# Performance work log

Measured on AMD Instinct MI355X. Metric: run time of the kernel, lower is better.

The kernel has to match this reference:

```python
import jax, jax.numpy as jnp
import numpy as np

NBIT = 8
QMAX = 2 ** (NBIT - 1) - 1  # 127, symmetric 8-bit range


def _sym_scale(x):
    # symmetric_linear_quantization_params: scale = max|x| / (2^(b-1)-1)
    return jnp.max(jnp.abs(x)) / QMAX


def setup_inputs() -> dict:
    key = jax.random.key(0)
    k1, k2, k3 = jax.random.split(key, 3)
    B, DIN, DOUT = 8192, 2048, 8192
    x = jax.random.normal(k1, (B, DIN), jnp.float32)
    weight = jax.random.normal(k2, (DOUT, DIN), jnp.float32) * 0.02
    bias = jax.random.normal(k3, (DOUT,), jnp.float32) * 0.01
    return {"x": x, "weight": weight, "bias": bias}


def reference(x, weight, bias):
    # --- QuantAct 1: symmetric 8-bit activation quantization ---
    s_a = _sym_scale(x)                                   # scalar act scale
    x_int = jnp.clip(jnp.round(x / s_a), -QMAX, QMAX)     # int8 values in fp32
    # --- QuantLinear: per-output-channel 8-bit weight quant + integer GEMM ---
    s_w = jnp.max(jnp.abs(weight), axis=1) / QMAX         # [DOUT] weight scales
    w_int = jnp.clip(jnp.round(weight / s_w[:, None]), -QMAX, QMAX)
    s_b = s_w * s_a                                        # output/bias scale [DOUT]
    b_int = jnp.round(bias / s_b)
    out_int = x_int @ w_int.T + b_int                      # [B, DOUT] int accumulation
    out = out_int * s_b                                    # dequantize
    # --- QuantAct 2: requantize output, symmetric 8-bit ---
    s_o = _sym_scale(out)
    out_q = jnp.clip(jnp.round(out / s_o), -QMAX, QMAX) * s_o
    return out_q
```

## Files before the change

### kernel.cpp

```cpp
#include <hip/hip_runtime.h>
#include <stdint.h>

#define B_DIM 8192
#define DIN   2048
#define DOUT  8192
#define NKT   (DIN / 128)

typedef int  v4i __attribute__((ext_vector_type(4)));
typedef char c8  __attribute__((ext_vector_type(8)));

__device__ __forceinline__ void gload_lds16(const void* g, void* l) {
  __builtin_amdgcn_global_load_lds(
      (const __attribute__((address_space(1))) void*)g,
      (__attribute__((address_space(3))) void*)l, 16, 0, 0);
}

__device__ __forceinline__ float wave_max(float m) {
#pragma unroll
  for (int off = 32; off; off >>= 1) m = fmaxf(m, __shfl_xor(m, off, 64));
  return m;
}

__global__ void k_init(unsigned int* p) {
  p[0] = 0u;
  p[1] = 0u;
}

__global__ __launch_bounds__(256) void k_absmax(const float4* __restrict__ x,
                                                int n4,
                                                unsigned int* __restrict__ out_bits) {
  int idx = blockIdx.x * blockDim.x + threadIdx.x;
  int stride = gridDim.x * blockDim.x;
  float m = 0.f;
  for (int i = idx; i < n4; i += stride) {
    float4 v = x[i];
    m = fmaxf(m, fabsf(v.x));
    m = fmaxf(m, fabsf(v.y));
    m = fmaxf(m, fabsf(v.z));
    m = fmaxf(m, fabsf(v.w));
  }
  m = wave_max(m);
  __shared__ float red[4];
  if ((threadIdx.x & 63) == 0) red[threadIdx.x >> 6] = m;
  __syncthreads();
  if (threadIdx.x == 0) {
    m = fmaxf(fmaxf(red[0], red[1]), fmaxf(red[2], red[3]));
    atomicMax(out_bits, __float_as_uint(m));
  }
}

__global__ void k_quant_x(const float* __restrict__ x, c8* __restrict__ xq,
                          int n8, const unsigned int* __restrict__ sa_bits) {
  int i = blockIdx.x * blockDim.x + threadIdx.x;
  if (i >= n8) return;
  float s_a = __uint_as_float(*sa_bits) / 127.0f;
  const float4* p = (const float4*)(x + (size_t)i * 8);
  float4 v0 = p[0], v1 = p[1];
  float vv[8] = {v0.x, v0.y, v0.z, v0.w, v1.x, v1.y, v1.z, v1.w};
  c8 q;
#pragma unroll
  for (int j = 0; j < 8; ++j) {
    float r = fminf(fmaxf(rintf(vv[j] / s_a), -127.f), 127.f);
    q[j] = (char)(int)r;
  }
  xq[i] = q;
}

__global__ __launch_bounds__(256) void k_quant_w(const float* __restrict__ w,
                                                 c8* __restrict__ wq,
                                                 float* __restrict__ s_w) {
  int row = blockIdx.x;
  int tid = threadIdx.x;
  const float4* wr = (const float4*)(w + (size_t)row * DIN);
  float4 v0 = wr[tid * 2], v1 = wr[tid * 2 + 1];
  float vv[8] = {v0.x, v0.y, v0.z, v0.w, v1.x, v1.y, v1.z, v1.w};
  float m = 0.f;
#pragma unroll
  for (int j = 0; j < 8; ++j) m = fmaxf(m, fabsf(vv[j]));
  m = wave_max(m);
  __shared__ float wmax[4];
  if ((tid & 63) == 0) wmax[tid >> 6] = m;
  __syncthreads();
  m = fmaxf(fmaxf(wmax[0], wmax[1]), fmaxf(wmax[2], wmax[3]));
  float s = m / 127.0f;
  if (tid == 0) s_w[row] = s;
  c8 q;
#pragma unroll
  for (int j = 0; j < 8; ++j) {
    float r = fminf(fmaxf(rintf(vv[j] / s), -127.f), 127.f);
    q[j] = (char)(int)r;
  }
  wq[(size_t)row * (DIN / 8) + tid] = q;
}

__global__ __launch_bounds__(512, 2) void k_gemm8(
    const char* __restrict__ Aq, const char* __restrict__ Bq,
    const float* __restrict__ s_w, const float* __restrict__ bias,
    const unsigned int* __restrict__ sa_bits, float* __restrict__ out,
    unsigned int* __restrict__ omax_bits) {
  __shared__ __align__(16) char lds[131072];

  const int tid = threadIdx.x;
  const int lane = tid & 63;
  const int wave = tid >> 6;
  const int wm = wave >> 2;
  const int wn = wave & 3;

  const int orig = blockIdx.x;
  const int xcd = orig & 7;
  const int k = orig >> 3;
  const int bx = (xcd & 3) * 8 + (k & 7);
  const int by = (xcd >> 2) * 16 + (k >> 3);
  const int row0 = by * 256, col0 = bx * 256;

  const int srow = ((tid >> 6) << 4) | (tid & 15);
  const int skb = tid & 48;
  const char* aS = Aq + (size_t)(row0 + srow) * DIN + skb;
  const char* bS = Bq + (size_t)(col0 + srow) * DIN + skb;

  auto STAGE = [&](int kt, int ks) {
    if (kt >= NKT) kt -= 2;
    int slot = kt & 1;
    const char* srcA = aS + (size_t)kt * 128 + ks * 64;
    const char* srcB = bS + (size_t)kt * 128 + ks * 64;
    int dstA = slot * 65536 + ks * 16384 + tid * 16;
    gload_lds16(srcA, &lds[dstA]);
    gload_lds16(srcA + (size_t)128 * DIN, &lds[dstA + 8192]);
    gload_lds16(srcB, &lds[dstA + 32768]);
    gload_lds16(srcB + (size_t)128 * DIN, &lds[dstA + 40960]);
  };

  v4i acc[2][4][4];
#pragma unroll
  for (int mh = 0; mh < 2; ++mh)
#pragma unroll
    for (int mf = 0; mf < 4; ++mf)
#pragma unroll
      for (int nf = 0; nf < 4; ++nf) acc[mh][mf][nf] = (v4i){0, 0, 0, 0};

  const int lb = lane * 16;
  v4i b0[4], al0[4], b1[4], al1[4];

#define PHASE(CSLOT, CKS, CUR_B, CUR_AL, NSLOT, NKS, NXT_B, NXT_AL, SKT, SKS) \
  do {                                                                        \
    asm volatile("s_waitcnt vmcnt(4)" ::: "memory");                          \
    asm volatile("s_barrier" ::: "memory");                                   \
    STAGE(SKT, SKS);                                                          \
    const int nb = (NSLOT)*65536 + (NKS)*16384;                               \
    _Pragma("unroll") for (int nf = 0; nf < 4; ++nf) NXT_B[nf] =              \
        *(const v4i*)&lds[nb + 32768 + (wn * 4 + nf) * 1024 + lb];            \
    _Pragma("unroll") for (int mf = 0; mf < 4; ++mf) NXT_AL[mf] =             \
        *(const v4i*)&lds[nb + (wm * 8 + mf) * 1024 + lb];                    \
    const int cb = (CSLOT)*65536 + (CKS)*16384;                               \
    v4i ah[4];                                                                \
    _Pragma("unroll") for (int mf = 0; mf < 4; ++mf) ah[mf] =                 \
        *(const v4i*)&lds[cb + (wm * 8 + 4 + mf) * 1024 + lb];                \
    __builtin_amdgcn_s_setprio(1);                                            \
    _Pragma("unroll") for (int mf = 0; mf < 4; ++mf)                          \
        _Pragma("unroll") for (int nf = 0; nf < 4; ++nf) acc[0][mf][nf] =     \
        __builtin_amdgcn_mfma_i32_16x16x64_i8(CUR_AL[mf], CUR_B[nf],          \
                                              acc[0][mf][nf], 0, 0, 0);       \
    _Pragma("unroll") for (int mf = 0; mf < 4; ++mf)                          \
        _Pragma("unroll") for (int nf = 0; nf < 4; ++nf) acc[1][mf][nf] =     \
        __builtin_amdgcn_mfma_i32_16x16x64_i8(ah[mf], CUR_B[nf],              \
                                              acc[1][mf][nf], 0, 0, 0);       \
    __builtin_amdgcn_s_setprio(0);                                            \
  } while (0)

  STAGE(0, 0);
  STAGE(0, 1);
  STAGE(1, 0);
  asm volatile("s_waitcnt vmcnt(8)" ::: "memory");
  asm volatile("s_barrier" ::: "memory");
#pragma unroll
  for (int nf = 0; nf < 4; ++nf)
    b0[nf] = *(const v4i*)&lds[32768 + (wn * 4 + nf) * 1024 + lb];
#pragma unroll
  for (int mf = 0; mf < 4; ++mf)
    al0[mf] = *(const v4i*)&lds[(wm * 8 + mf) * 1024 + lb];

#pragma unroll 1
  for (int i = 0; i < NKT / 2; ++i) {
    PHASE(0, 0, b0, al0, 0, 1, b1, al1, 2 * i + 1, 1);
    PHASE(0, 1, b1, al1, 1, 0, b0, al0, 2 * i + 2, 0);
    PHASE(1, 0, b0, al0, 1, 1, b1, al1, 2 * i + 2, 1);
    PHASE(1, 1, b1, al1, 0, 0, b0, al0, 2 * i + 3, 0);
  }
#undef PHASE

  const int fr = lane & 15;
  float s_a = __uint_as_float(*sa_bits) / 127.0f;
  float lmax = 0.f;
#pragma unroll
  for (int nf = 0; nf < 4; ++nf) {
    int col = col0 + wn * 64 + nf * 16 + fr;
    float sw = s_w[col];
    float sb = sw * s_a;
    float bint = rintf(bias[col] / sb);
#pragma unroll
    for (int mh = 0; mh < 2; ++mh)
#pragma unroll
      for (int mf = 0; mf < 4; ++mf) {
        int rbase = row0 + wm * 128 + mh * 64 + mf * 16 + (lane >> 4) * 4;
#pragma unroll
        for (int r = 0; r < 4; ++r) {
          float o = ((float)acc[mh][mf][nf][r] + bint) * sb;
          out[(size_t)(rbase + r) * DOUT + col] = o;
          lmax = fmaxf(lmax, fabsf(o));
        }
      }
  }
  lmax = wave_max(lmax);
  asm volatile("s_waitcnt vmcnt(0)" ::: "memory");
  __syncthreads();
  float* red = (float*)lds;
  if (lane == 0) red[wave] = lmax;
  __syncthreads();
  if (tid == 0) {
    float m = 0.f;
#pragma unroll
    for (int w2 = 0; w2 < 8; ++w2) m = fmaxf(m, red[w2]);
    atomicMax(omax_bits, __float_as_uint(m));
  }
}

__global__ void k_requant(float4* __restrict__ out, int n4,
                          const unsigned int* __restrict__ omax_bits) {
  float s_o = __uint_as_float(*omax_bits) / 127.0f;
  int idx = blockIdx.x * blockDim.x + threadIdx.x;
  int stride = gridDim.x * blockDim.x;
  for (int i = idx; i < n4; i += stride) {
    float4 v = out[i];
    v.x = fminf(fmaxf(rintf(v.x / s_o), -127.f), 127.f) * s_o;
    v.y = fminf(fmaxf(rintf(v.y / s_o), -127.f), 127.f) * s_o;
    v.z = fminf(fmaxf(rintf(v.z / s_o), -127.f), 127.f) * s_o;
    v.w = fminf(fmaxf(rintf(v.w / s_o), -127.f), 127.f) * s_o;
    out[i] = v;
  }
}

extern "C" void kernel_launch(void* const* d_in, const int* in_sizes, int n_in,
                              void* d_out, int out_size, void* d_ws,
                              size_t ws_size, hipStream_t stream) {
  const float* x = (const float*)d_in[0];
  const float* w = (const float*)d_in[1];
  const float* bias = (const float*)d_in[2];
  float* out = (float*)d_out;
  char* ws = (char*)d_ws;

  unsigned int* absbits = (unsigned int*)ws;
  float* s_w = (float*)(ws + 512);
  char* xq = ws + 65536;
  char* wq = ws + 65536 + (size_t)B_DIM * DIN;

  k_init<<<1, 1, 0, stream>>>(absbits);
  k_absmax<<<1024, 256, 0, stream>>>((const float4*)x, B_DIM * DIN / 4, absbits);
  k_quant_x<<<(B_DIM * DIN / 8) / 256, 256, 0, stream>>>(x, (c8*)xq,
                                                         B_DIM * DIN / 8, absbits);
  k_quant_w<<<DOUT, 256, 0, stream>>>(w, (c8*)wq, s_w);
  k_gemm8<<<1024, 512, 0, stream>>>(xq, wq, s_w, bias, absbits, out, absbits + 1);
  k_requant<<<4096, 256, 0, stream>>>((float4*)out, B_DIM * DOUT / 4, absbits + 1);
}
```

Before: 345.6 us.

## Replace pipelined 256x256 int8 GEMM with simple single-buffered 128x128 tile kernel

The hand-pipelined, double-buffered 256x256-tile int8 GEMM is replaced with a plain 128x128-tile kernel of 256 threads and a 32KB LDS buffer. Each k-step loads into LDS, synchronises, then runs the MFMAs, with no overlap between loads and compute. The intent is to raise occupancy and simplify scheduling, but it loses the software pipelining and halves data reuse per tile, which raises global traffic and adds barrier stalls.

```diff
diff --git a/kernel.cpp b/kernel.cpp
--- a/kernel.cpp
+++ b/kernel.cpp
@@ -93,100 +93,71 @@
   wq[(size_t)row * (DIN / 8) + tid] = q;
 }
 
-__global__ __launch_bounds__(512, 2) void k_gemm8(
+__global__ __launch_bounds__(256, 3) void k_gemm(
     const char* __restrict__ Aq, const char* __restrict__ Bq,
     const float* __restrict__ s_w, const float* __restrict__ bias,
     const unsigned int* __restrict__ sa_bits, float* __restrict__ out,
     unsigned int* __restrict__ omax_bits) {
-  __shared__ __align__(16) char lds[131072];
+  __shared__ __align__(16) char lds[32768];
 
   const int tid = threadIdx.x;
   const int lane = tid & 63;
   const int wave = tid >> 6;
-  const int wm = wave >> 2;
-  const int wn = wave & 3;
+  const int wm = wave >> 1;
+  const int wn = wave & 1;
 
   const int orig = blockIdx.x;
   const int xcd = orig & 7;
   const int k = orig >> 3;
-  const int bx = (xcd & 3) * 8 + (k & 7);
-  const int by = (xcd >> 2) * 16 + (k >> 3);
-  const int row0 = by * 256, col0 = bx * 256;
+  const int bx = (xcd & 3) * 16 + (k & 15);
+  const int by = (xcd >> 2) * 32 + (k >> 4);
+  const int row0 = by * 128, col0 = bx * 128;
 
   const int srow = ((tid >> 6) << 4) | (tid & 15);
   const int skb = tid & 48;
   const char* aS = Aq + (size_t)(row0 + srow) * DIN + skb;
   const char* bS = Bq + (size_t)(col0 + srow) * DIN + skb;
 
-  auto STAGE = [&](int kt, int ks) {
-    if (kt >= NKT) kt -= 2;
-    int slot = kt & 1;
-    const char* srcA = aS + (size_t)kt * 128 + ks * 64;
-    const char* srcB = bS + (size_t)kt * 128 + ks * 64;
-    int dstA = slot * 65536 + ks * 16384 + tid * 16;
-    gload_lds16(srcA, &lds[dstA]);
-    gload_lds16(srcA + (size_t)128 * DIN, &lds[dstA + 8192]);
-    gload_lds16(srcB, &lds[dstA + 32768]);
-    gload_lds16(srcB + (size_t)128 * DIN, &lds[dstA + 40960]);
-  };
-
-  v4i acc[2][4][4];
-#pragma unroll
-  for (int mh = 0; mh < 2; ++mh)
-#pragma unroll
-    for (int mf = 0; mf < 4; ++mf)
-#pragma unroll
-      for (int nf = 0; nf < 4; ++nf) acc[mh][mf][nf] = (v4i){0, 0, 0, 0};
+  v4i acc[4][4];
+#pragma unroll
+  for (int mf = 0; mf < 4; ++mf)
+#pragma unroll
+    for (int nf = 0; nf < 4; ++nf) acc[mf][nf] = (v4i){0, 0, 0, 0};
 
   const int lb = lane * 16;
-  v4i b0[4], al0[4], b1[4], al1[4];
-
-#define PHASE(CSLOT, CKS, CUR_B, CUR_AL, NSLOT, NKS, NXT_B, NXT_AL, SKT, SKS) \
-  do {                                                                        \
-    asm volatile("s_waitcnt vmcnt(4)" ::: "memory");                          \
-    asm volatile("s_barrier" ::: "memory");                                   \
-    STAGE(SKT, SKS);                                                          \
-    const int nb = (NSLOT)*65536 + (NKS)*16384;                               \
-    _Pragma("unroll") for (int nf = 0; nf < 4; ++nf) NXT_B[nf] =              \
-        *(const v4i*)&lds[nb + 32768 + (wn * 4 + nf) * 1024 + lb];            \
-    _Pragma("unroll") for (int mf = 0; mf < 4; ++mf) NXT_AL[mf] =             \
-        *(const v4i*)&lds[nb + (wm * 8 + mf) * 1024 + lb];                    \
-    const int cb = (CSLOT)*65536 + (CKS)*16384;                               \
-    v4i ah[4];                                                                \
-    _Pragma("unroll") for (int mf = 0; mf < 4; ++mf) ah[mf] =                 \
-        *(const v4i*)&lds[cb + (wm * 8 + 4 + mf) * 1024 + lb];                \
-    __builtin_amdgcn_s_setprio(1);                                            \
-    _Pragma("unroll") for (int mf = 0; mf < 4; ++mf)                          \
-        _Pragma("unroll") for (int nf = 0; nf < 4; ++nf) acc[0][mf][nf] =     \
-        __builtin_amdgcn_mfma_i32_16x16x64_i8(CUR_AL[mf], CUR_B[nf],          \
-                                              acc[0][mf][nf], 0, 0, 0);       \
-    _Pragma("unroll") for (int mf = 0; mf < 4; ++mf)                          \
-        _Pragma("unroll") for (int nf = 0; nf < 4; ++nf) acc[1][mf][nf] =     \
-        __builtin_amdgcn_mfma_i32_16x16x64_i8(ah[mf], CUR_B[nf],              \
-                                              acc[1][mf][nf], 0, 0, 0);       \
-    __builtin_amdgcn_s_setprio(0);                                            \
-  } while (0)
-
-  STAGE(0, 0);
-  STAGE(0, 1);
-  STAGE(1, 0);
-  asm volatile("s_waitcnt vmcnt(8)" ::: "memory");
-  asm volatile("s_barrier" ::: "memory");
-#pragma unroll
-  for (int nf = 0; nf < 4; ++nf)
-    b0[nf] = *(const v4i*)&lds[32768 + (wn * 4 + nf) * 1024 + lb];
-#pragma unroll
-  for (int mf = 0; mf < 4; ++mf)
-    al0[mf] = *(const v4i*)&lds[(wm * 8 + mf) * 1024 + lb];
 
 #pragma unroll 1
-  for (int i = 0; i < NKT / 2; ++i) {
-    PHASE(0, 0, b0, al0, 0, 1, b1, al1, 2 * i + 1, 1);
-    PHASE(0, 1, b1, al1, 1, 0, b0, al0, 2 * i + 2, 0);
-    PHASE(1, 0, b0, al0, 1, 1, b1, al1, 2 * i + 2, 1);
-    PHASE(1, 1, b1, al1, 0, 0, b0, al0, 2 * i + 3, 0);
-  }
-#undef PHASE
+  for (int kt = 0; kt < NKT; ++kt) {
+    __syncthreads();
+    const char* srcA = aS + (size_t)kt * 128;
+    const char* srcB = bS + (size_t)kt * 128;
+#pragma unroll
+    for (int ks = 0; ks < 2; ++ks) {
+      const int d = ks * 8192 + tid * 16;
+      gload_lds16(srcA + ks * 64, &lds[d]);
+      gload_lds16(srcA + (size_t)64 * DIN + ks * 64, &lds[d + 4096]);
+      gload_lds16(srcB + ks * 64, &lds[16384 + d]);
+      gload_lds16(srcB + (size_t)64 * DIN + ks * 64, &lds[16384 + d + 4096]);
+    }
+    __syncthreads();
+
+#pragma unroll
+    for (int ks = 0; ks < 2; ++ks) {
+      v4i a_[4], b_[4];
+      const int ab = ks * 8192 + (wm * 4) * 1024 + lb;
+      const int bb = 16384 + ks * 8192 + (wn * 4) * 1024 + lb;
+#pragma unroll
+      for (int mf = 0; mf < 4; ++mf) a_[mf] = *(const v4i*)&lds[ab + mf * 1024];
+#pragma unroll
+      for (int nf = 0; nf < 4; ++nf) b_[nf] = *(const v4i*)&lds[bb + nf * 1024];
+#pragma unroll
+      for (int nf = 0; nf < 4; ++nf)
+#pragma unroll
+        for (int mf = 0; mf < 4; ++mf)
+          acc[mf][nf] = __builtin_amdgcn_mfma_i32_16x16x64_i8(
+              a_[mf], b_[nf], acc[mf][nf], 0, 0, 0);
+    }
+  }
 
   const int fr = lane & 15;
   float s_a = __uint_as_float(*sa_bits) / 127.0f;
@@ -198,28 +169,23 @@
     float sb = sw * s_a;
     float bint = rintf(bias[col] / sb);
 #pragma unroll
-    for (int mh = 0; mh < 2; ++mh)
-#pragma unroll
-      for (int mf = 0; mf < 4; ++mf) {
-        int rbase = row0 + wm * 128 + mh * 64 + mf * 16 + (lane >> 4) * 4;
-#pragma unroll
-        for (int r = 0; r < 4; ++r) {
-          float o = ((float)acc[mh][mf][nf][r] + bint) * sb;
-          out[(size_t)(rbase + r) * DOUT + col] = o;
-          lmax = fmaxf(lmax, fabsf(o));
-        }
+    for (int mf = 0; mf < 4; ++mf) {
+      int rbase = row0 + wm * 64 + mf * 16 + (lane >> 4) * 4;
+#pragma unroll
+      for (int r = 0; r < 4; ++r) {
+        float o = ((float)acc[mf][nf][r] + bint) * sb;
+        out[(size_t)(rbase + r) * DOUT + col] = o;
+        lmax = fmaxf(lmax, fabsf(o));
       }
+    }
   }
   lmax = wave_max(lmax);
-  asm volatile("s_waitcnt vmcnt(0)" ::: "memory");
   __syncthreads();
   float* red = (float*)lds;
   if (lane == 0) red[wave] = lmax;
   __syncthreads();
   if (tid == 0) {
-    float m = 0.f;
-#pragma unroll
-    for (int w2 = 0; w2 < 8; ++w2) m = fmaxf(m, red[w2]);
+    float m = fmaxf(fmaxf(red[0], red[1]), fmaxf(red[2], red[3]));
     atomicMax(omax_bits, __float_as_uint(m));
   }
 }
@@ -258,6 +224,6 @@
   k_quant_x<<<(B_DIM * DIN / 8) / 256, 256, 0, stream>>>(x, (c8*)xq,
                                                          B_DIM * DIN / 8, absbits);
   k_quant_w<<<DOUT, 256, 0, stream>>>(w, (c8*)wq, s_w);
-  k_gemm8<<<1024, 512, 0, stream>>>(xq, wq, s_w, bias, absbits, out, absbits + 1);
+  k_gemm<<<4096, 256, 0, stream>>>(xq, wq, s_w, bias, absbits, out, absbits + 1);
   k_requant<<<4096, 256, 0, stream>>>((float4*)out, B_DIM * DOUT / 4, absbits + 1);
 }
```

Result: slower. 421.7 us (+22.0%).
